# Performance work log

Measured on AMD Instinct MI355X. Metric: run time of the kernel, lower is better.

The kernel has to match this reference:

```python
import jax, jax.numpy as jnp
import numpy as np

EPS = 1e-12
SHRINK = 0.0025

def _l2norm(x, axis=1):
    return x / jnp.maximum(jnp.linalg.norm(x, axis=axis, keepdims=True), EPS)

def setup_inputs() -> dict:
    key = jax.random.key(0)
    ks = jax.random.split(key, 6)
    N, C, H, W = 32, 512, 32, 32
    mem_dim, spatial = 512, H * W
    hid = spatial // 2
    x = jax.random.normal(ks[0], (N, C, H, W), dtype=jnp.float32)
    memory = jax.random.normal(ks[1], (mem_dim, spatial), dtype=jnp.float32)
    memory = _l2norm(memory, axis=1)  # buffer is L2-normalized at init
    w1 = jax.random.normal(ks[2], (hid, spatial), dtype=jnp.float32) * 0.02
    b1 = jax.random.normal(ks[3], (hid,), dtype=jnp.float32) * 0.02
    w2 = jax.random.normal(ks[4], (spatial, hid), dtype=jnp.float32) * 0.02
    b2 = jax.random.normal(ks[5], (spatial,), dtype=jnp.float32) * 0.02
    return {"x": x, "memory": memory, "w1": w1, "b1": b1, "w2": w2, "b2": b2}

def reference(x, memory, w1, b1, w2, b2):
    N, C, H, W = x.shape
    mem_dim = memory.shape[0]
    input_flat = x.reshape(N * C, H * W)
    input_norm = _l2norm(input_flat, axis=1)
    # shared MLP over memory bank: Linear -> ReLU -> Linear -> ReLU
    h = jax.nn.relu(memory @ w1.T + b1)
    mem_proc = jax.nn.relu(h @ w2.T + b2)
    memory_norm = _l2norm(mem_proc, axis=1)
    # addressing: cosine sim -> softmax -> hard shrink -> L1 renorm
    att = jax.nn.softmax(input_norm @ memory_norm.T, axis=1)  # [N*C, M]
    att = jax.nn.relu(att - SHRINK)
    att = att / jnp.maximum(att.sum(axis=1, keepdims=True), EPS)  # p=1 norm (att >= 0)
    output = (att @ memory_norm).reshape(N, C, H, W)
    att_channel_avg = att.reshape(N, C, mem_dim).mean(axis=1)  # [N, M]
    att_spatial = jnp.broadcast_to(att_channel_avg[:, :, None, None], (N, mem_dim, H, W))
    return output, att_spatial, input_flat, memory_norm, att
```

## Files before the change

kernel.cpp:

```cpp
#include <hip/hip_runtime.h>

typedef float  f32x4  __attribute__((ext_vector_type(4)));
typedef __bf16 bf16x8 __attribute__((ext_vector_type(8)));
typedef __bf16 bf16x4 __attribute__((ext_vector_type(4)));

#define L2EPS   1e-12f
#define SHRINKC 0.0025f


__device__ __forceinline__ bf16x8 pack_bf16(f32x4 v0, f32x4 v1) {
  bf16x8 r;
  r[0] = (__bf16)v0[0]; r[1] = (__bf16)v0[1]; r[2] = (__bf16)v0[2]; r[3] = (__bf16)v0[3];
  r[4] = (__bf16)v1[0]; r[5] = (__bf16)v1[1]; r[6] = (__bf16)v1[2]; r[7] = (__bf16)v1[3];
  return r;
}

__device__ __forceinline__ bf16x8 load_cvt_bf16x8(const float* p) {
  const f32x4* q = (const f32x4*)p;
  return pack_bf16(q[0], q[1]);
}

__device__ __forceinline__ float dot4(f32x4 v) {
  return v[0]*v[0] + v[1]*v[1] + v[2]*v[2] + v[3]*v[3];
}

__global__ __launch_bounds__(64) void gemm_bt_bias_relu(
    const float* __restrict__ A, const float* __restrict__ B,
    const float* __restrict__ bias, float* __restrict__ C,
    int M, int N, int K) {
  const int r0   = blockIdx.x * 32;
  const int n0   = blockIdx.y * 32;
  const int lane = threadIdx.x & 63;
  const int quad = lane >> 4;
  const int m    = lane & 15;

  f32x4 acc[2][2] = {};
  for (int k0 = 0; k0 < K; k0 += 32) {
    const int kk = k0 + quad * 8;
    bf16x8 a[2], b[2];
    #pragma unroll
    for (int rg = 0; rg < 2; ++rg)
      a[rg] = load_cvt_bf16x8(A + (size_t)(r0 + rg * 16 + m) * K + kk);
    #pragma unroll
    for (int cf = 0; cf < 2; ++cf)
      b[cf] = load_cvt_bf16x8(B + (size_t)(n0 + cf * 16 + m) * K + kk);
    #pragma unroll
    for (int rg = 0; rg < 2; ++rg)
      #pragma unroll
      for (int cf = 0; cf < 2; ++cf)
        acc[rg][cf] = __builtin_amdgcn_mfma_f32_16x16x32_bf16(a[rg], b[cf], acc[rg][cf], 0, 0, 0);
  }
  #pragma unroll
  for (int rg = 0; rg < 2; ++rg)
    #pragma unroll
    for (int cf = 0; cf < 2; ++cf) {
      const int n = n0 + cf * 16 + m;
      const float bv = bias[n];
      #pragma unroll
      for (int vi = 0; vi < 4; ++vi) {
        const int r = r0 + rg * 16 + quad * 4 + vi;
        C[(size_t)r * N + n] = fmaxf(acc[rg][cf][vi] + bv, 0.f);
      }
    }
}

__global__ __launch_bounds__(256) void norm_rows(
    const float* __restrict__ mp, float* __restrict__ mn_f32,
    __bf16* __restrict__ mn_bf16) {
  const int r = blockIdx.x;
  const int tid = threadIdx.x;
  const f32x4 v = *(const f32x4*)(mp + (size_t)r * 1024 + tid * 4);
  float ss = dot4(v);
  #pragma unroll
  for (int d = 1; d < 64; d <<= 1) ss += __shfl_xor(ss, d);
  __shared__ float wsum[4];
  __shared__ float invs;
  if ((tid & 63) == 0) wsum[tid >> 6] = ss;
  __syncthreads();
  if (tid == 0) {
    float t = wsum[0] + wsum[1] + wsum[2] + wsum[3];
    invs = 1.f / fmaxf(sqrtf(t), L2EPS);
  }
  __syncthreads();
  const float iv = invs;
  f32x4 o = v * iv;
  *(f32x4*)(mn_f32 + (size_t)r * 1024 + tid * 4) = o;
  bf16x4 ob;
  ob[0] = (__bf16)o[0]; ob[1] = (__bf16)o[1]; ob[2] = (__bf16)o[2]; ob[3] = (__bf16)o[3];
  *(bf16x4*)(mn_bf16 + (size_t)r * 1024 + tid * 4) = ob;
}

__global__ __launch_bounds__(256) void attend(
    const float* __restrict__ x, const __bf16* __restrict__ Mn,
    const float* __restrict__ Mnf, float* __restrict__ out_flat,
    float* __restrict__ out_out, float* __restrict__ out_att,
    float* __restrict__ attsum) {
  __shared__ float S[32][512];
  __shared__ float invn[32];
  const int r0   = blockIdx.x * 32;
  const int tid  = threadIdx.x;
  const int wave = tid >> 6;
  const int lane = tid & 63;
  const int quad = lane >> 4;
  const int m    = lane & 15;
  const int n0w  = wave * 128;

  float ss0 = 0.f, ss1 = 0.f;
  f32x4 acc[8][2] = {};
  for (int k0 = 0; k0 < 1024; k0 += 32) {
    const int kk = k0 + quad * 8;
    bf16x8 a[2];
    f32x4 v0a, v0b, v1a, v1b;
    {
      const int row = r0 + m;
      const f32x4* q = (const f32x4*)(x + (size_t)row * 1024 + kk);
      v0a = q[0]; v0b = q[1];
      a[0] = pack_bf16(v0a, v0b);
      ss0 += dot4(v0a) + dot4(v0b);
    }
    {
      const int row = r0 + 16 + m;
      const f32x4* q = (const f32x4*)(x + (size_t)row * 1024 + kk);
      v1a = q[0]; v1b = q[1];
      a[1] = pack_bf16(v1a, v1b);
      ss1 += dot4(v1a) + dot4(v1b);
    }
    if (wave == 0) {
      float* d0 = out_flat + (size_t)(r0 + m) * 1024 + kk;
      float* d1 = out_flat + (size_t)(r0 + 16 + m) * 1024 + kk;
      *(f32x4*)d0 = v0a; *(f32x4*)(d0 + 4) = v0b;
      *(f32x4*)d1 = v1a; *(f32x4*)(d1 + 4) = v1b;
    }
    #pragma unroll
    for (int nf = 0; nf < 8; ++nf) {
      const bf16x8 b = *(const bf16x8*)(Mn + (size_t)(n0w + nf * 16 + m) * 1024 + kk);
      acc[nf][0] = __builtin_amdgcn_mfma_f32_16x16x32_bf16(a[0], b, acc[nf][0], 0, 0, 0);
      acc[nf][1] = __builtin_amdgcn_mfma_f32_16x16x32_bf16(a[1], b, acc[nf][1], 0, 0, 0);
    }
  }
  ss0 += __shfl_xor(ss0, 16); ss0 += __shfl_xor(ss0, 32);
  ss1 += __shfl_xor(ss1, 16); ss1 += __shfl_xor(ss1, 32);
  if (wave == 0 && quad == 0) {
    invn[m]      = 1.f / fmaxf(sqrtf(ss0), L2EPS);
    invn[16 + m] = 1.f / fmaxf(sqrtf(ss1), L2EPS);
  }
  #pragma unroll
  for (int nf = 0; nf < 8; ++nf)
    #pragma unroll
    for (int rg = 0; rg < 2; ++rg)
      #pragma unroll
      for (int vi = 0; vi < 4; ++vi)
        S[rg * 16 + quad * 4 + vi][n0w + nf * 16 + m] = acc[nf][rg][vi];
  __syncthreads();

  const int row = tid >> 3;
  const int sub = tid & 7;
  const float iv = invn[row];
  float mx = -1e30f;
  for (int i = 0; i < 64; ++i) {
    const int c = (sub + 4 * row + 8 * i) & 511;
    mx = fmaxf(mx, S[row][c]);
  }
  #pragma unroll
  for (int d = 1; d < 8; d <<= 1) mx = fmaxf(mx, __shfl_xor(mx, d));
  float se = 0.f;
  for (int i = 0; i < 64; ++i) {
    const int c = (sub + 4 * row + 8 * i) & 511;
    se += __expf((S[row][c] - mx) * iv);
  }
  #pragma unroll
  for (int d = 1; d < 8; d <<= 1) se += __shfl_xor(se, d);
  const float inv_se = 1.f / se;
  float rsum = 0.f;
  for (int i = 0; i < 64; ++i) {
    const int c = (sub + 4 * row + 8 * i) & 511;
    const float sh = fmaxf(__expf((S[row][c] - mx) * iv) * inv_se - SHRINKC, 0.f);
    S[row][c] = sh;
    rsum += sh;
  }
  #pragma unroll
  for (int d = 1; d < 8; d <<= 1) rsum += __shfl_xor(rsum, d);
  const float invr = 1.f / fmaxf(rsum, L2EPS);
  for (int i = 0; i < 64; ++i) {
    const int c = (sub + 4 * row + 8 * i) & 511;
    S[row][c] *= invr;
  }
  const int any = __syncthreads_or((sub == 0) && (rsum > 0.f));

  {
    float* dst = out_att + (size_t)r0 * 512;
    for (int idx = tid; idx < 32 * 512 / 4; idx += 256) {
      const int f = idx * 4;
      *(f32x4*)(dst + f) = *(const f32x4*)(&S[f >> 9][f & 511]);
    }
  }

  if (!any) {
    const f32x4 z = {0.f, 0.f, 0.f, 0.f};
    float* dst = out_out + (size_t)r0 * 1024;
    for (int idx = tid; idx < 32 * 1024 / 4; idx += 256)
      *(f32x4*)(dst + idx * 4) = z;
  } else {
    const int nimg = r0 >> 9;
    for (int c = tid; c < 512; c += 256) {
      float s = 0.f;
      for (int rr = 0; rr < 32; ++rr) s += S[rr][c];
      atomicAdd(&attsum[nimg * 512 + c], s);
    }
    const int c0 = tid * 4;
    for (int rr = 0; rr < 32; ++rr) {
      f32x4 o = {0.f, 0.f, 0.f, 0.f};
      for (int mm = 0; mm < 512; ++mm) {
        const float a = S[rr][mm];
        o += a * (*(const f32x4*)(Mnf + (size_t)mm * 1024 + c0));
      }
      *(f32x4*)(out_out + (size_t)(r0 + rr) * 1024 + c0) = o;
    }
  }
}

__global__ __launch_bounds__(256) void spread(
    const float* __restrict__ attsum, float* __restrict__ out_sp) {
  const int nm = blockIdx.x;
  const float v = attsum[nm] * (1.f / 512.f);
  const f32x4 vv = {v, v, v, v};
  *(f32x4*)(out_sp + (size_t)nm * 1024 + threadIdx.x * 4) = vv;
}


extern "C" void kernel_launch(void* const* d_in, const int* in_sizes, int n_in,
                              void* d_out, int out_size, void* d_ws, size_t ws_size,
                              hipStream_t stream) {
  const float* x      = (const float*)d_in[0];
  const float* memory = (const float*)d_in[1];
  const float* w1     = (const float*)d_in[2];
  const float* b1     = (const float*)d_in[3];
  const float* w2     = (const float*)d_in[4];
  const float* b2     = (const float*)d_in[5];

  float* out = (float*)d_out;
  float* out_output = out;
  float* out_attsp  = out + 16777216;
  float* out_flat   = out + 33554432;
  float* out_mnorm  = out + 50331648;
  float* out_att    = out + 50855936;

  char* ws = (char*)d_ws;
  float*  h      = (float*)ws;
  float*  mp     = (float*)(ws + (1 << 20));
  __bf16* mnb    = (__bf16*)(ws + (1 << 20) + (2 << 20));
  float*  attsum = (float*)(ws + (1 << 20) + (2 << 20) + (1 << 20));

  hipMemsetAsync(attsum, 0, 32 * 512 * sizeof(float), stream);

  gemm_bt_bias_relu<<<dim3(16, 16), 64, 0, stream>>>(memory, w1, b1, h, 512, 512, 1024);
  gemm_bt_bias_relu<<<dim3(16, 32), 64, 0, stream>>>(h, w2, b2, mp, 512, 1024, 512);
  norm_rows<<<512, 256, 0, stream>>>(mp, out_mnorm, mnb);
  attend<<<512, 256, 0, stream>>>(x, mnb, out_mnorm, out_flat, out_output, out_att, attsum);
  spread<<<16384, 256, 0, stream>>>(attsum, out_attsp);
}
```

Before: 419.3 us.

## Fuse second MLP GEMM with row L2-norm and fold memset into first GEMM

```diff
diff --git a/kernel.cpp b/kernel.cpp
--- a/kernel.cpp
+++ b/kernel.cpp
@@ -24,10 +24,14 @@
   return v[0]*v[0] + v[1]*v[1] + v[2]*v[2] + v[3]*v[3];
 }
 
-__global__ __launch_bounds__(64) void gemm_bt_bias_relu(
+__global__ __launch_bounds__(64) void gemm1(
     const float* __restrict__ A, const float* __restrict__ B,
     const float* __restrict__ bias, float* __restrict__ C,
-    int M, int N, int K) {
+    float* __restrict__ attsum) {
+  const int bid = blockIdx.y * gridDim.x + blockIdx.x;
+  attsum[bid * 64 + threadIdx.x] = 0.f;
+
+  const int K = 1024, N = 512;
   const int r0   = blockIdx.x * 32;
   const int n0   = blockIdx.y * 32;
   const int lane = threadIdx.x & 63;
@@ -64,30 +68,69 @@
     }
 }
 
-__global__ __launch_bounds__(256) void norm_rows(
-    const float* __restrict__ mp, float* __restrict__ mn_f32,
-    __bf16* __restrict__ mn_bf16) {
-  const int r = blockIdx.x;
-  const int tid = threadIdx.x;
-  const f32x4 v = *(const f32x4*)(mp + (size_t)r * 1024 + tid * 4);
-  float ss = dot4(v);
-  #pragma unroll
-  for (int d = 1; d < 64; d <<= 1) ss += __shfl_xor(ss, d);
-  __shared__ float wsum[4];
-  __shared__ float invs;
-  if ((tid & 63) == 0) wsum[tid >> 6] = ss;
+__global__ __launch_bounds__(256) void gemm2_norm(
+    const float* __restrict__ A,
+    const float* __restrict__ B,
+    const float* __restrict__ bias,
+    float* __restrict__ mn_f32, __bf16* __restrict__ mn_bf16) {
+  const int r0   = blockIdx.x * 16;
+  const int wave = threadIdx.x >> 6;
+  const int lane = threadIdx.x & 63;
+  const int quad = lane >> 4;
+  const int m    = lane & 15;
+  const int n0   = wave * 256;
+
+  f32x4 acc[16] = {};
+  for (int k0 = 0; k0 < 512; k0 += 32) {
+    const int kk = k0 + quad * 8;
+    const bf16x8 a = load_cvt_bf16x8(A + (size_t)(r0 + m) * 512 + kk);
+    #pragma unroll
+    for (int cf = 0; cf < 16; ++cf) {
+      const bf16x8 b = load_cvt_bf16x8(B + (size_t)(n0 + cf * 16 + m) * 512 + kk);
+      acc[cf] = __builtin_amdgcn_mfma_f32_16x16x32_bf16(a, b, acc[cf], 0, 0, 0);
+    }
+  }
+  float ss[4] = {0.f, 0.f, 0.f, 0.f};
+  #pragma unroll
+  for (int cf = 0; cf < 16; ++cf) {
+    const float bv = bias[n0 + cf * 16 + m];
+    #pragma unroll
+    for (int vi = 0; vi < 4; ++vi) {
+      const float v = fmaxf(acc[cf][vi] + bv, 0.f);
+      acc[cf][vi] = v;
+      ss[vi] += v * v;
+    }
+  }
+  #pragma unroll
+  for (int vi = 0; vi < 4; ++vi)
+    #pragma unroll
+    for (int d = 1; d < 16; d <<= 1) ss[vi] += __shfl_xor(ss[vi], d);
+
+  __shared__ float psum[4][16];
+  __shared__ float invs[16];
+  if (m == 0) {
+    #pragma unroll
+    for (int vi = 0; vi < 4; ++vi) psum[wave][quad * 4 + vi] = ss[vi];
+  }
   __syncthreads();
-  if (tid == 0) {
-    float t = wsum[0] + wsum[1] + wsum[2] + wsum[3];
-    invs = 1.f / fmaxf(sqrtf(t), L2EPS);
+  if (threadIdx.x < 16) {
+    const float t = psum[0][threadIdx.x] + psum[1][threadIdx.x] +
+                    psum[2][threadIdx.x] + psum[3][threadIdx.x];
+    invs[threadIdx.x] = 1.f / fmaxf(sqrtf(t), L2EPS);
   }
   __syncthreads();
-  const float iv = invs;
-  f32x4 o = v * iv;
-  *(f32x4*)(mn_f32 + (size_t)r * 1024 + tid * 4) = o;
-  bf16x4 ob;
-  ob[0] = (__bf16)o[0]; ob[1] = (__bf16)o[1]; ob[2] = (__bf16)o[2]; ob[3] = (__bf16)o[3];
-  *(bf16x4*)(mn_bf16 + (size_t)r * 1024 + tid * 4) = ob;
+  #pragma unroll
+  for (int vi = 0; vi < 4; ++vi) {
+    const int r = r0 + quad * 4 + vi;
+    const float iv = invs[quad * 4 + vi];
+    #pragma unroll
+    for (int cf = 0; cf < 16; ++cf) {
+      const int n = n0 + cf * 16 + m;
+      const float o = acc[cf][vi] * iv;
+      mn_f32[(size_t)r * 1024 + n] = o;
+      mn_bf16[(size_t)r * 1024 + n] = (__bf16)o;
+    }
+  }
 }
 
 __global__ __launch_bounds__(256) void attend(
@@ -247,15 +290,11 @@
 
   char* ws = (char*)d_ws;
   float*  h      = (float*)ws;
-  float*  mp     = (float*)(ws + (1 << 20));
-  __bf16* mnb    = (__bf16*)(ws + (1 << 20) + (2 << 20));
-  float*  attsum = (float*)(ws + (1 << 20) + (2 << 20) + (1 << 20));
-
-  hipMemsetAsync(attsum, 0, 32 * 512 * sizeof(float), stream);
-
-  gemm_bt_bias_relu<<<dim3(16, 16), 64, 0, stream>>>(memory, w1, b1, h, 512, 512, 1024);
-  gemm_bt_bias_relu<<<dim3(16, 32), 64, 0, stream>>>(h, w2, b2, mp, 512, 1024, 512);
-  norm_rows<<<512, 256, 0, stream>>>(mp, out_mnorm, mnb);
+  __bf16* mnb    = (__bf16*)(ws + (1 << 20));
+  float*  attsum = (float*)(ws + (1 << 20) + (1 << 20));
+
+  gemm1<<<dim3(16, 16), 64, 0, stream>>>(memory, w1, b1, h, attsum);
+  gemm2_norm<<<32, 256, 0, stream>>>(h, w2, b2, out_mnorm, mnb);
   attend<<<512, 256, 0, stream>>>(x, mnb, out_mnorm, out_flat, out_output, out_att, attsum);
   spread<<<16384, 256, 0, stream>>>(attsum, out_attsp);
 }
```

Result: slower. 464.6 us (+10.8%).
